# Kernel tuning notes

Hardware: AMD Instinct MI355X
Metric: run time of the kernel (lower is better)

The kernel has to match this reference:

```python
import jax, jax.numpy as jnp
import numpy as np

WEIGHT = 1.0

def _saturation(x):
    # x: (B,3,H,W) in [-1,1] -> RGB in [0,1] -> HSV saturation channel (B,H,W)
    rgb = (x + 1.0) * 0.5
    v = jnp.max(rgb, axis=1)
    mn = jnp.min(rgb, axis=1)
    delta = v - mn
    # skimage rgb2hsv: S = delta / max, with S = 0 where max == 0
    safe_v = jnp.where(v > 0, v, 1.0)
    return jnp.where(v > 0, delta / safe_v, 0.0)


def setup_inputs() -> dict:
    key = jax.random.key(0)
    k1, k2 = jax.random.split(key)
    shape = (32, 3, 512, 512)
    # uniform in [-1, 1], matching the module's expected input range
    generated = jax.random.uniform(k1, shape, dtype=jnp.float32) * 2.0 - 1.0
    target = jax.random.uniform(k2, shape, dtype=jnp.float32) * 2.0 - 1.0
    return {"generated": generated, "target": target}


def reference(generated, target):
    s_gen = _saturation(generated)
    s_tgt = _saturation(target)
    loss = jnp.mean(jnp.abs(s_gen - s_tgt))  # F.l1_loss default 'mean'
    return WEIGHT * loss
```

## Files before the change

### kernel.cpp

```cpp
#include <hip/hip_runtime.h>

#define HW      (512 * 512)
#define NBATCH  32
#define NPIX    (NBATCH * HW)
#define NGROUP  (NPIX / 4)
#define NBLOCKS 2048
#define NTHREADS 256

__device__ __forceinline__ float saturation(float x_r, float x_g, float x_b) {
    float r = (x_r + 1.0f) * 0.5f;
    float g = (x_g + 1.0f) * 0.5f;
    float b = (x_b + 1.0f) * 0.5f;
    float v  = fmaxf(fmaxf(r, g), b);
    float mn = fminf(fminf(r, g), b);
    float d  = v - mn;
    return (v > 0.0f) ? (d / v) : 0.0f;
}

__global__ __launch_bounds__(NTHREADS) void sat_loss_partial(
        const float* __restrict__ gen,
        const float* __restrict__ tgt,
        float* __restrict__ partial) {
    const int tid = blockIdx.x * blockDim.x + threadIdx.x;
    const int stride = gridDim.x * blockDim.x;

    float acc = 0.0f;
    for (int g = tid; g < NGROUP; g += stride) {
        const int b = g >> 16;
        const long r = (long)(g & 65535) << 2;
        const long base = (long)b * (3L * HW) + r;

        const float4 ar = *(const float4*)(gen + base);
        const float4 ag = *(const float4*)(gen + base + HW);
        const float4 ab = *(const float4*)(gen + base + 2L * HW);
        const float4 br = *(const float4*)(tgt + base);
        const float4 bg = *(const float4*)(tgt + base + HW);
        const float4 bb = *(const float4*)(tgt + base + 2L * HW);

        acc += fabsf(saturation(ar.x, ag.x, ab.x) - saturation(br.x, bg.x, bb.x));
        acc += fabsf(saturation(ar.y, ag.y, ab.y) - saturation(br.y, bg.y, bb.y));
        acc += fabsf(saturation(ar.z, ag.z, ab.z) - saturation(br.z, bg.z, bb.z));
        acc += fabsf(saturation(ar.w, ag.w, ab.w) - saturation(br.w, bg.w, bb.w));
    }

    #pragma unroll
    for (int off = 32; off > 0; off >>= 1)
        acc += __shfl_down(acc, off, 64);

    __shared__ float wave_sum[NTHREADS / 64];
    const int lane = threadIdx.x & 63;
    const int wid  = threadIdx.x >> 6;
    if (lane == 0) wave_sum[wid] = acc;
    __syncthreads();

    if (threadIdx.x == 0) {
        float s = 0.0f;
        #pragma unroll
        for (int i = 0; i < NTHREADS / 64; ++i) s += wave_sum[i];
        partial[blockIdx.x] = s;
    }
}

__global__ __launch_bounds__(NTHREADS) void sat_loss_finalize(
        const float* __restrict__ partial,
        float* __restrict__ out) {
    float acc = 0.0f;
    for (int i = threadIdx.x; i < NBLOCKS; i += NTHREADS)
        acc += partial[i];

    #pragma unroll
    for (int off = 32; off > 0; off >>= 1)
        acc += __shfl_down(acc, off, 64);

    __shared__ float wave_sum[NTHREADS / 64];
    const int lane = threadIdx.x & 63;
    const int wid  = threadIdx.x >> 6;
    if (lane == 0) wave_sum[wid] = acc;
    __syncthreads();

    if (threadIdx.x == 0) {
        float s = 0.0f;
        #pragma unroll
        for (int i = 0; i < NTHREADS / 64; ++i) s += wave_sum[i];
        out[0] = s * (1.0f / (float)NPIX);
    }
}

extern "C" void kernel_launch(void* const* d_in, const int* in_sizes, int n_in,
                              void* d_out, int out_size, void* d_ws, size_t ws_size,
                              hipStream_t stream) {
    const float* gen = (const float*)d_in[0];
    const float* tgt = (const float*)d_in[1];
    float* out = (float*)d_out;
    float* partial = (float*)d_ws;

    sat_loss_partial<<<NBLOCKS, NTHREADS, 0, stream>>>(gen, tgt, partial);
    sat_loss_finalize<<<1, NTHREADS, 0, stream>>>(partial, out);
}
```

Baseline: 38.89 us.

## Replace grid-stride loop with fixed two-group-per-thread loads and simplify saturation math

Drops the grid-stride loop. The grid doubles to 4096 blocks and each thread handles exactly two 4-pixel groups, issuing all twelve float4 loads up front so more memory requests are in flight at once. The saturation computation works on the raw [-1,1] values: it takes max and min, then divides (max-min) by (max+1), which avoids the per-channel affine transform. The design hardcodes the thread-to-work mapping for this exact problem size, and using more registers per thread may reduce occupancy.

```diff
diff --git a/kernel.cpp b/kernel.cpp
--- a/kernel.cpp
+++ b/kernel.cpp
@@ -1,47 +1,58 @@
 #include <hip/hip_runtime.h>
 
-#define HW      (512 * 512)
-#define NBATCH  32
-#define NPIX    (NBATCH * HW)
-#define NGROUP  (NPIX / 4)
-#define NBLOCKS 2048
+#define HW       (512 * 512)
+#define NBATCH   32
+#define NPIX     (NBATCH * HW)
+#define NGROUP   (NPIX / 4)
+#define NBLOCKS  4096
 #define NTHREADS 256
+#define TOTAL_T  (NBLOCKS * NTHREADS)
 
-__device__ __forceinline__ float saturation(float x_r, float x_g, float x_b) {
-    float r = (x_r + 1.0f) * 0.5f;
-    float g = (x_g + 1.0f) * 0.5f;
-    float b = (x_b + 1.0f) * 0.5f;
-    float v  = fmaxf(fmaxf(r, g), b);
+__device__ __forceinline__ float sat_raw(float r, float g, float b) {
+    float mx = fmaxf(fmaxf(r, g), b);
     float mn = fminf(fminf(r, g), b);
-    float d  = v - mn;
-    return (v > 0.0f) ? (d / v) : 0.0f;
+    float vp = mx + 1.0f;
+    return (vp > 0.0f) ? ((mx - mn) / vp) : 0.0f;
+}
+
+__device__ __forceinline__ float sat_diff4(
+        const float4& ar, const float4& ag, const float4& ab,
+        const float4& br, const float4& bg, const float4& bb) {
+    float s = 0.0f;
+    s += fabsf(sat_raw(ar.x, ag.x, ab.x) - sat_raw(br.x, bg.x, bb.x));
+    s += fabsf(sat_raw(ar.y, ag.y, ab.y) - sat_raw(br.y, bg.y, bb.y));
+    s += fabsf(sat_raw(ar.z, ag.z, ab.z) - sat_raw(br.z, bg.z, bb.z));
+    s += fabsf(sat_raw(ar.w, ag.w, ab.w) - sat_raw(br.w, bg.w, bb.w));
+    return s;
 }
 
 __global__ __launch_bounds__(NTHREADS) void sat_loss_partial(
         const float* __restrict__ gen,
         const float* __restrict__ tgt,
         float* __restrict__ partial) {
-    const int tid = blockIdx.x * blockDim.x + threadIdx.x;
-    const int stride = gridDim.x * blockDim.x;
+    const int tid = blockIdx.x * NTHREADS + threadIdx.x;
 
-    float acc = 0.0f;
-    for (int g = tid; g < NGROUP; g += stride) {
-        const int b = g >> 16;
-        const long r = (long)(g & 65535) << 2;
-        const long base = (long)b * (3L * HW) + r;
+    const int g0 = tid;
+    const int g1 = tid + TOTAL_T;
 
-        const float4 ar = *(const float4*)(gen + base);
-        const float4 ag = *(const float4*)(gen + base + HW);
-        const float4 ab = *(const float4*)(gen + base + 2L * HW);
-        const float4 br = *(const float4*)(tgt + base);
-        const float4 bg = *(const float4*)(tgt + base + HW);
-        const float4 bb = *(const float4*)(tgt + base + 2L * HW);
+    const long base0 = (long)(g0 >> 16) * (3L * HW) + ((long)(g0 & 65535) << 2);
+    const long base1 = (long)(g1 >> 16) * (3L * HW) + ((long)(g1 & 65535) << 2);
 
-        acc += fabsf(saturation(ar.x, ag.x, ab.x) - saturation(br.x, bg.x, bb.x));
-        acc += fabsf(saturation(ar.y, ag.y, ab.y) - saturation(br.y, bg.y, bb.y));
-        acc += fabsf(saturation(ar.z, ag.z, ab.z) - saturation(br.z, bg.z, bb.z));
-        acc += fabsf(saturation(ar.w, ag.w, ab.w) - saturation(br.w, bg.w, bb.w));
-    }
+    const float4 a0r = *(const float4*)(gen + base0);
+    const float4 a0g = *(const float4*)(gen + base0 + HW);
+    const float4 a0b = *(const float4*)(gen + base0 + 2L * HW);
+    const float4 b0r = *(const float4*)(tgt + base0);
+    const float4 b0g = *(const float4*)(tgt + base0 + HW);
+    const float4 b0b = *(const float4*)(tgt + base0 + 2L * HW);
+    const float4 a1r = *(const float4*)(gen + base1);
+    const float4 a1g = *(const float4*)(gen + base1 + HW);
+    const float4 a1b = *(const float4*)(gen + base1 + 2L * HW);
+    const float4 b1r = *(const float4*)(tgt + base1);
+    const float4 b1g = *(const float4*)(tgt + base1 + HW);
+    const float4 b1b = *(const float4*)(tgt + base1 + 2L * HW);
+
+    float acc = sat_diff4(a0r, a0g, a0b, b0r, b0g, b0b)
+              + sat_diff4(a1r, a1g, a1b, b1r, b1g, b1b);
 
     #pragma unroll
     for (int off = 32; off > 0; off >>= 1)
```

Result: no change. 39.55 us (+1.7%).

## Fuse finalize into main kernel via fixed-point atomics and last-block completion

Applied to the files above, without the earlier changes.

Replaces the second reduction kernel with a fixed-point 64-bit atomic accumulation plus a completion counter, so the last block writes the mean. It also fully unrolls the grid-stride loop to four fixed iterations and simplifies the saturation math by folding the (x+1)/2 rescale into the ratio. The intent is to remove one kernel launch and the partial-array round trip. In exchange it adds a hipMemsetAsync per call, global atomics, and rounding error from converting each block sum to fixed point.

```diff
diff --git a/kernel.cpp b/kernel.cpp
--- a/kernel.cpp
+++ b/kernel.cpp
@@ -1,31 +1,32 @@
 #include <hip/hip_runtime.h>
 
-#define HW      (512 * 512)
-#define NBATCH  32
-#define NPIX    (NBATCH * HW)
-#define NGROUP  (NPIX / 4)
-#define NBLOCKS 2048
+#define HW       (512 * 512)
+#define NPIX     (32 * HW)
+#define NGROUP   (NPIX / 4)
+#define NBLOCKS  2048
 #define NTHREADS 256
+#define TOTAL_T  (NBLOCKS * NTHREADS)
+#define SCALE    2097152.0f
 
-__device__ __forceinline__ float saturation(float x_r, float x_g, float x_b) {
-    float r = (x_r + 1.0f) * 0.5f;
-    float g = (x_g + 1.0f) * 0.5f;
-    float b = (x_b + 1.0f) * 0.5f;
-    float v  = fmaxf(fmaxf(r, g), b);
+__device__ __forceinline__ float sat_raw(float r, float g, float b) {
+    float mx = fmaxf(fmaxf(r, g), b);
     float mn = fminf(fminf(r, g), b);
-    float d  = v - mn;
-    return (v > 0.0f) ? (d / v) : 0.0f;
+    float vp = mx + 1.0f;
+    return (vp > 0.0f) ? ((mx - mn) / vp) : 0.0f;
 }
 
-__global__ __launch_bounds__(NTHREADS) void sat_loss_partial(
+__global__ __launch_bounds__(NTHREADS) void sat_loss_fused(
         const float* __restrict__ gen,
         const float* __restrict__ tgt,
-        float* __restrict__ partial) {
-    const int tid = blockIdx.x * blockDim.x + threadIdx.x;
-    const int stride = gridDim.x * blockDim.x;
+        unsigned long long* __restrict__ acc,
+        unsigned int* __restrict__ count,
+        float* __restrict__ out) {
+    const int tid = blockIdx.x * NTHREADS + threadIdx.x;
 
-    float acc = 0.0f;
-    for (int g = tid; g < NGROUP; g += stride) {
+    float s = 0.0f;
+    #pragma unroll
+    for (int k = 0; k < 4; ++k) {
+        const int g = tid + k * TOTAL_T;
         const int b = g >> 16;
         const long r = (long)(g & 65535) << 2;
         const long base = (long)b * (3L * HW) + r;
@@ -37,52 +38,36 @@
         const float4 bg = *(const float4*)(tgt + base + HW);
         const float4 bb = *(const float4*)(tgt + base + 2L * HW);
 
-        acc += fabsf(saturation(ar.x, ag.x, ab.x) - saturation(br.x, bg.x, bb.x));
-        acc += fabsf(saturation(ar.y, ag.y, ab.y) - saturation(br.y, bg.y, bb.y));
-        acc += fabsf(saturation(ar.z, ag.z, ab.z) - saturation(br.z, bg.z, bb.z));
-        acc += fabsf(saturation(ar.w, ag.w, ab.w) - saturation(br.w, bg.w, bb.w));
+        s += fabsf(sat_raw(ar.x, ag.x, ab.x) - sat_raw(br.x, bg.x, bb.x));
+        s += fabsf(sat_raw(ar.y, ag.y, ab.y) - sat_raw(br.y, bg.y, bb.y));
+        s += fabsf(sat_raw(ar.z, ag.z, ab.z) - sat_raw(br.z, bg.z, bb.z));
+        s += fabsf(sat_raw(ar.w, ag.w, ab.w) - sat_raw(br.w, bg.w, bb.w));
     }
 
     #pragma unroll
     for (int off = 32; off > 0; off >>= 1)
-        acc += __shfl_down(acc, off, 64);
+        s += __shfl_down(s, off, 64);
 
     __shared__ float wave_sum[NTHREADS / 64];
     const int lane = threadIdx.x & 63;
     const int wid  = threadIdx.x >> 6;
-    if (lane == 0) wave_sum[wid] = acc;
+    if (lane == 0) wave_sum[wid] = s;
     __syncthreads();
 
     if (threadIdx.x == 0) {
-        float s = 0.0f;
+        float bsum = 0.0f;
         #pragma unroll
-        for (int i = 0; i < NTHREADS / 64; ++i) s += wave_sum[i];
-        partial[blockIdx.x] = s;
-    }
-}
+        for (int i = 0; i < NTHREADS / 64; ++i) bsum += wave_sum[i];
 
-__global__ __launch_bounds__(NTHREADS) void sat_loss_finalize(
-        const float* __restrict__ partial,
-        float* __restrict__ out) {
-    float acc = 0.0f;
-    for (int i = threadIdx.x; i < NBLOCKS; i += NTHREADS)
-        acc += partial[i];
-
-    #pragma unroll
-    for (int off = 32; off > 0; off >>= 1)
-        acc += __shfl_down(acc, off, 64);
-
-    __shared__ float wave_sum[NTHREADS / 64];
-    const int lane = threadIdx.x & 63;
-    const int wid  = threadIdx.x >> 6;
-    if (lane == 0) wave_sum[wid] = acc;
-    __syncthreads();
-
-    if (threadIdx.x == 0) {
-        float s = 0.0f;
-        #pragma unroll
-        for (int i = 0; i < NTHREADS / 64; ++i) s += wave_sum[i];
-        out[0] = s * (1.0f / (float)NPIX);
+        const unsigned long long fx = (unsigned long long)llrintf(bsum * SCALE);
+        atomicAdd(acc, fx);
+        __threadfence();
+        const unsigned int prev = atomicAdd(count, 1u);
+        if (prev == NBLOCKS - 1) {
+            __threadfence();
+            const unsigned long long total = atomicAdd(acc, 0ULL);
+            out[0] = (float)((double)total * (1.0 / (double)SCALE) / (double)NPIX);
+        }
     }
 }
 
@@ -92,8 +77,10 @@
     const float* gen = (const float*)d_in[0];
     const float* tgt = (const float*)d_in[1];
     float* out = (float*)d_out;
-    float* partial = (float*)d_ws;
+    unsigned long long* acc = (unsigned long long*)d_ws;
+    unsigned int* count = (unsigned int*)((char*)d_ws + 8);
 
-    sat_loss_partial<<<NBLOCKS, NTHREADS, 0, stream>>>(gen, tgt, partial);
-    sat_loss_finalize<<<1, NTHREADS, 0, stream>>>(partial, out);
+    hipMemsetAsync(d_ws, 0, 16, stream);
+
+    sat_loss_fused<<<NBLOCKS, NTHREADS, 0, stream>>>(gen, tgt, acc, count, out);
 }
```

Result: slower. 102.1 us (+162.6%).
